# Kernel optimization log

Measured on AMD Instinct MI355X. Metric: run time of the kernel, lower is better.

## Reference

```python
import jax, jax.numpy as jnp
import numpy as np

BATCH, NODES, ENC, DEC = 8192, 1_000_000, 128, 128


def setup_inputs() -> dict:
    key = jax.random.key(0)
    k1, k2, k3, k4 = jax.random.split(key, 4)
    query = jax.random.normal(k1, (BATCH, DEC), dtype=jnp.float32)
    values = jax.random.normal(k2, (NODES, ENC), dtype=jnp.float32)
    index = jax.random.randint(k3, (NODES,), 0, BATCH)
    W = jax.random.uniform(k4, (DEC, ENC), dtype=jnp.float32)
    return {"query": query, "values": values, "index": index, "W": W}


def reference(query, values, index, W):
    # query: [B, Ddec], values: [N, Denc], index: [N] in [0, B), W: [Ddec, Denc]
    batch = query.shape[0]
    dec = W.shape[0]
    # Original computes scores = query @ (W @ values.T) -> [B, N], then
    # scatter_softmax per segment along nodes, then gathers weights[index[n], n].
    # Only the row index[n] of column n is ever used, so we compute exactly
    # those entries: s[n] = <query[index[n]] @ W, values[n]> / sqrt(dec).
    qW = query @ W                                   # [B, Denc]
    s = jnp.einsum("ne,ne->n", qW[index], values)    # [N]
    s = s / jnp.sqrt(jnp.asarray(dec, dtype=s.dtype))
    # segment-wise stable softmax over nodes within each segment
    smax = jax.ops.segment_max(s, index, num_segments=batch)   # [B]
    e = jnp.exp(s - smax[index])                               # [N]
    denom = jax.ops.segment_sum(e, index, num_segments=batch)  # [B]
    w = e / denom[index]                                       # [N]
    # weighted scatter-add pooling -> [B, Denc]
    return jax.ops.segment_sum(w[:, None] * values, index, num_segments=batch)
```

## Files before the change

kernel.cpp:

```cpp
#include <hip/hip_runtime.h>
#include <hip/hip_bf16.h>
#include <cmath>

#define ENCD 128
#define DECD 128
#define CHUNK 8

__global__ void init_counts(int* __restrict__ counts, int B) {
    int i = blockIdx.x * blockDim.x + threadIdx.x;
    if (i < B) counts[i] = 0;
}

__global__ void qw_gemm(const float* __restrict__ query, const float* __restrict__ W,
                        float* __restrict__ qW) {
    __shared__ float qs[8][DECD];
    const int t = threadIdx.x;
    const int row0 = blockIdx.x * 8;
    for (int i = t; i < 8 * DECD; i += 256)
        qs[i >> 7][i & 127] = query[(size_t)row0 * DECD + i];
    __syncthreads();
    const int c = t & 127;
    const int rh = t >> 7;
    float a0 = 0.f, a1 = 0.f, a2 = 0.f, a3 = 0.f;
    for (int k = 0; k < DECD; ++k) {
        const float w = W[k * ENCD + c];
        a0 += qs[rh * 4 + 0][k] * w;
        a1 += qs[rh * 4 + 1][k] * w;
        a2 += qs[rh * 4 + 2][k] * w;
        a3 += qs[rh * 4 + 3][k] * w;
    }
    qW[(size_t)(row0 + rh * 4 + 0) * ENCD + c] = a0;
    qW[(size_t)(row0 + rh * 4 + 1) * ENCD + c] = a1;
    qW[(size_t)(row0 + rh * 4 + 2) * ENCD + c] = a2;
    qW[(size_t)(row0 + rh * 4 + 3) * ENCD + c] = a3;
}

__global__ void hist_kernel(const int* __restrict__ index, int* __restrict__ counts, int N) {
    int n = blockIdx.x * blockDim.x + threadIdx.x;
    if (n < N) atomicAdd(&counts[index[n]], 1);
}

__global__ void scan_kernel(const int* __restrict__ counts, int* __restrict__ offsets,
                            int* __restrict__ cursor, int B) {
    __shared__ int tot[1024];
    const int t = threadIdx.x;
    int local[8];
    int s = 0;
#pragma unroll
    for (int i = 0; i < 8; ++i) {
        const int ci = t * 8 + i;
        local[i] = (ci < B) ? counts[ci] : 0;
        s += local[i];
    }
    tot[t] = s;
    __syncthreads();
    for (int off = 1; off < 1024; off <<= 1) {
        int v = (t >= off) ? tot[t - off] : 0;
        __syncthreads();
        tot[t] += v;
        __syncthreads();
    }
    int excl = tot[t] - s;
#pragma unroll
    for (int i = 0; i < 8; ++i) {
        const int ci = t * 8 + i;
        if (ci < B) { offsets[ci] = excl; cursor[ci] = excl; }
        excl += local[i];
    }
    if (t == 1023) offsets[B] = tot[1023];
}

__global__ void scatter_kernel(const int* __restrict__ index, int* __restrict__ cursor,
                               int* __restrict__ nodeids, int N) {
    int n = blockIdx.x * blockDim.x + threadIdx.x;
    if (n < N) {
        const int p = atomicAdd(&cursor[index[n]], 1);
        nodeids[p] = n;
    }
}

__global__ __launch_bounds__(128) void seg_attn(
    const float* __restrict__ values, const float* __restrict__ qW,
    const int* __restrict__ offsets, const int* __restrict__ nodeids,
    float* __restrict__ out) {
    const int b = blockIdx.x;
    const int t = threadIdx.x;
    const int beg = offsets[b];
    const int cnt = offsets[b + 1] - beg;

    __shared__ float qsh[ENCD];
    __shared__ float vrow[CHUNK][ENCD + 4];
    __shared__ float s_sh[CHUNK];
    __shared__ int   nid_sh[CHUNK];

    qsh[t] = qW[(size_t)b * ENCD + t];
    __syncthreads();

    const int g  = t & 15;
    const int jn = t >> 4;
    float qreg[8];
#pragma unroll
    for (int i = 0; i < 8; ++i) qreg[i] = qsh[g * 8 + i];

    float m = -INFINITY, l = 0.f, acc = 0.f;
    const float inv_sqrt_d = 0.08838834764831845f;

    for (int base = 0; base < cnt; base += CHUNK) {
        const int nim = min(CHUNK, cnt - base);
        if (t < CHUNK) nid_sh[t] = nodeids[beg + ((t < nim) ? (base + t) : base)];
        __syncthreads();

        {
            const int r0 = t >> 5;
            const int c4 = (t & 31) * 4;
#pragma unroll
            for (int it = 0; it < 2; ++it) {
                const int r = r0 + it * 4;
                const float4 v = *(const float4*)(values + (size_t)nid_sh[r] * ENCD + c4);
                *(float4*)&vrow[r][c4] = v;
            }
        }
        __syncthreads();

        float pd = 0.f;
#pragma unroll
        for (int i = 0; i < 8; ++i) pd += qreg[i] * vrow[jn][g * 8 + i];
        pd += __shfl_xor(pd, 1);
        pd += __shfl_xor(pd, 2);
        pd += __shfl_xor(pd, 4);
        pd += __shfl_xor(pd, 8);
        if (g == 0) s_sh[jn] = (jn < nim) ? pd * inv_sqrt_d : -INFINITY;
        __syncthreads();

        float sv[CHUNK];
        float m_ch = -INFINITY;
#pragma unroll
        for (int j = 0; j < CHUNK; ++j) { sv[j] = s_sh[j]; m_ch = fmaxf(m_ch, sv[j]); }
        const float m_new = fmaxf(m, m_ch);
        const float scale = __expf(m - m_new);
        float psum = 0.f, accadd = 0.f;
#pragma unroll
        for (int j = 0; j < CHUNK; ++j) {
            const float p = __expf(sv[j] - m_new);
            psum += p;
            accadd += p * vrow[j][t];
        }
        l = l * scale + psum;
        acc = acc * scale + accadd;
        m = m_new;
    }

    out[(size_t)b * ENCD + t] = (l > 0.f) ? (acc / l) : 0.f;
}

extern "C" void kernel_launch(void* const* d_in, const int* in_sizes, int n_in,
                              void* d_out, int out_size, void* d_ws, size_t ws_size,
                              hipStream_t stream) {
    const float* query  = (const float*)d_in[0];
    const float* values = (const float*)d_in[1];
    const int*   index  = (const int*)d_in[2];
    const float* W      = (const float*)d_in[3];
    float* out = (float*)d_out;

    const int B = in_sizes[0] / DECD;
    const int N = in_sizes[2];

    float* qW      = (float*)d_ws;
    int*   nodeids = (int*)(qW + (size_t)B * ENCD);
    int*   counts  = nodeids + N;
    int*   offsets = counts + B;
    int*   cursor  = offsets + B + 1;

    init_counts<<<(B + 255) / 256, 256, 0, stream>>>(counts, B);
    qw_gemm<<<B / 8, 256, 0, stream>>>(query, W, qW);
    hist_kernel<<<(N + 255) / 256, 256, 0, stream>>>(index, counts, N);
    scan_kernel<<<1, 1024, 0, stream>>>(counts, offsets, cursor, B);
    scatter_kernel<<<(N + 255) / 256, 256, 0, stream>>>(index, cursor, nodeids, N);
    seg_attn<<<B, 128, 0, stream>>>(values, qW, offsets, nodeids, out);
}
```

Measured before the change: 845.0 us.

## Widen segment attention to 256 threads with 32-node chunks and vectorize histogram

The segment attention kernel now runs 256 threads per segment and stages 32 node rows per chunk instead of 8. Two thread halves each accumulate the softmax-weighted sum over 16 rows and merge their partial results through shared memory at the end. The aim is to cut the number of chunk iterations and barriers per segment and to keep more gather loads in flight. The histogram kernel now reads four indices per thread with an int4 load. The cost is larger per-chunk padding waste on small segments and more shared memory per block.

```diff
diff --git a/kernel.cpp b/kernel.cpp
--- a/kernel.cpp
+++ b/kernel.cpp
@@ -4,7 +4,7 @@
 
 #define ENCD 128
 #define DECD 128
-#define CHUNK 8
+#define CHUNK 32
 
 __global__ void init_counts(int* __restrict__ counts, int B) {
     int i = blockIdx.x * blockDim.x + threadIdx.x;
@@ -36,8 +36,16 @@
 }
 
 __global__ void hist_kernel(const int* __restrict__ index, int* __restrict__ counts, int N) {
-    int n = blockIdx.x * blockDim.x + threadIdx.x;
-    if (n < N) atomicAdd(&counts[index[n]], 1);
+    int n4 = (blockIdx.x * blockDim.x + threadIdx.x) * 4;
+    if (n4 + 3 < N) {
+        const int4 v = *(const int4*)(index + n4);
+        atomicAdd(&counts[v.x], 1);
+        atomicAdd(&counts[v.y], 1);
+        atomicAdd(&counts[v.z], 1);
+        atomicAdd(&counts[v.w], 1);
+    } else {
+        for (int n = n4; n < N; ++n) atomicAdd(&counts[index[n]], 1);
+    }
 }
 
 __global__ void scan_kernel(const int* __restrict__ counts, int* __restrict__ offsets,
@@ -79,7 +87,7 @@
     }
 }
 
-__global__ __launch_bounds__(128) void seg_attn(
+__global__ __launch_bounds__(256) void seg_attn(
     const float* __restrict__ values, const float* __restrict__ qW,
     const int* __restrict__ offsets, const int* __restrict__ nodeids,
     float* __restrict__ out) {
@@ -92,8 +100,10 @@
     __shared__ float vrow[CHUNK][ENCD + 4];
     __shared__ float s_sh[CHUNK];
     __shared__ int   nid_sh[CHUNK];
-
-    qsh[t] = qW[(size_t)b * ENCD + t];
+    __shared__ float mrg_a[ENCD];
+    __shared__ float mrg_l[ENCD];
+
+    if (t < ENCD) qsh[t] = qW[(size_t)b * ENCD + t];
     __syncthreads();
 
     const int g  = t & 15;
@@ -102,6 +112,9 @@
 #pragma unroll
     for (int i = 0; i < 8; ++i) qreg[i] = qsh[g * 8 + i];
 
+    const int col  = t & 127;
+    const int half = t >> 7;
+
     float m = -INFINITY, l = 0.f, acc = 0.f;
     const float inv_sqrt_d = 0.08838834764831845f;
 
@@ -114,43 +127,53 @@
             const int r0 = t >> 5;
             const int c4 = (t & 31) * 4;
 #pragma unroll
-            for (int it = 0; it < 2; ++it) {
-                const int r = r0 + it * 4;
+            for (int it = 0; it < 4; ++it) {
+                const int r = r0 + it * 8;
                 const float4 v = *(const float4*)(values + (size_t)nid_sh[r] * ENCD + c4);
                 *(float4*)&vrow[r][c4] = v;
             }
         }
         __syncthreads();
 
-        float pd = 0.f;
-#pragma unroll
-        for (int i = 0; i < 8; ++i) pd += qreg[i] * vrow[jn][g * 8 + i];
-        pd += __shfl_xor(pd, 1);
-        pd += __shfl_xor(pd, 2);
-        pd += __shfl_xor(pd, 4);
-        pd += __shfl_xor(pd, 8);
-        if (g == 0) s_sh[jn] = (jn < nim) ? pd * inv_sqrt_d : -INFINITY;
-        __syncthreads();
-
-        float sv[CHUNK];
+#pragma unroll
+        for (int p = 0; p < 2; ++p) {
+            const int j = jn + p * 16;
+            float pd = 0.f;
+#pragma unroll
+            for (int i = 0; i < 8; ++i) pd += qreg[i] * vrow[j][g * 8 + i];
+            pd += __shfl_xor(pd, 1);
+            pd += __shfl_xor(pd, 2);
+            pd += __shfl_xor(pd, 4);
+            pd += __shfl_xor(pd, 8);
+            if (g == 0) s_sh[j] = (j < nim) ? pd * inv_sqrt_d : -INFINITY;
+        }
+        __syncthreads();
+
         float m_ch = -INFINITY;
 #pragma unroll
-        for (int j = 0; j < CHUNK; ++j) { sv[j] = s_sh[j]; m_ch = fmaxf(m_ch, sv[j]); }
+        for (int j = 0; j < CHUNK; ++j) m_ch = fmaxf(m_ch, s_sh[j]);
         const float m_new = fmaxf(m, m_ch);
         const float scale = __expf(m - m_new);
         float psum = 0.f, accadd = 0.f;
 #pragma unroll
-        for (int j = 0; j < CHUNK; ++j) {
-            const float p = __expf(sv[j] - m_new);
+        for (int jj = 0; jj < 16; ++jj) {
+            const int j = half * 16 + jj;
+            const float p = __expf(s_sh[j] - m_new);
             psum += p;
-            accadd += p * vrow[j][t];
+            accadd += p * vrow[j][col];
         }
         l = l * scale + psum;
         acc = acc * scale + accadd;
         m = m_new;
     }
 
-    out[(size_t)b * ENCD + t] = (l > 0.f) ? (acc / l) : 0.f;
+    if (half == 1) { mrg_a[col] = acc; mrg_l[col] = l; }
+    __syncthreads();
+    if (half == 0) {
+        const float at = acc + mrg_a[col];
+        const float lt = l + mrg_l[col];
+        out[(size_t)b * ENCD + col] = (lt > 0.f) ? (at / lt) : 0.f;
+    }
 }
 
 extern "C" void kernel_launch(void* const* d_in, const int* in_sizes, int n_in,
@@ -173,8 +196,8 @@
 
     init_counts<<<(B + 255) / 256, 256, 0, stream>>>(counts, B);
     qw_gemm<<<B / 8, 256, 0, stream>>>(query, W, qW);
-    hist_kernel<<<(N + 255) / 256, 256, 0, stream>>>(index, counts, N);
+    hist_kernel<<<(N / 4 + 255) / 256, 256, 0, stream>>>(index, counts, N);
     scan_kernel<<<1, 1024, 0, stream>>>(counts, offsets, cursor, B);
     scatter_kernel<<<(N + 255) / 256, 256, 0, stream>>>(index, cursor, nodeids, N);
-    seg_attn<<<B, 128, 0, stream>>>(values, qW, offsets, nodeids, out);
-}
+    seg_attn<<<B, 256, 0, stream>>>(values, qW, offsets, nodeids, out);
+}
```

New measurement: 837.7 us. Within noise of the previous version (-0.9%).
